# Performance work log

Hardware: AMD Instinct MI355X
Metric: run time of the kernel (lower is better)

## Reference

```python
import jax, jax.numpy as jnp
import numpy as np

N = 100000   # nodes
E = 1600000  # edges
F = 128      # n_feat
HID = 64     # n_hid
L = 4        # n_layer
C = 40       # n_class
TEMP = 0.1   # summarize temperature


def setup_inputs() -> dict:
    key = jax.random.key(0)
    ks = jax.random.split(key, 10)
    x = jax.random.normal(ks[0], (N, F), dtype=jnp.float32)
    edge_index = jax.random.randint(ks[1], (2, E), 0, N, dtype=jnp.int64)
    s_in = 1.0 / np.sqrt(F)
    s_h = 1.0 / np.sqrt(HID)
    W0 = jax.random.normal(ks[2], (F, HID), dtype=jnp.float32) * s_in
    b0 = jnp.zeros((HID,), dtype=jnp.float32)
    Ws = jax.random.normal(ks[3], (L - 1, HID, HID), dtype=jnp.float32) * s_h
    bs = jnp.zeros((L - 1, HID), dtype=jnp.float32)
    Wq = jax.random.normal(ks[4], (HID, HID), dtype=jnp.float32) * s_h
    Wk = jax.random.normal(ks[5], (HID, HID), dtype=jnp.float32) * s_h
    Wout = jax.random.normal(ks[6], (HID, C), dtype=jnp.float32) * s_h
    bout = jnp.zeros((C,), dtype=jnp.float32)
    return {"x": x, "edge_index": edge_index, "W0": W0, "b0": b0,
            "Ws": Ws, "bs": bs, "Wq": Wq, "Wk": Wk, "Wout": Wout, "bout": bout}


def reference(x, edge_index, W0, b0, Ws, bs, Wq, Wk, Wout, bout):
    # --- GCN normalization with self-loops (symmetric D^-1/2 (A+I) D^-1/2) ---
    loop = jnp.arange(N, dtype=edge_index.dtype)
    src = jnp.concatenate([edge_index[0], loop])  # [E+N]
    dst = jnp.concatenate([edge_index[1], loop])
    deg = jax.ops.segment_sum(jnp.ones_like(dst, dtype=x.dtype), dst, num_segments=N)
    dinv = jnp.where(deg > 0, jax.lax.rsqrt(deg), 0.0)
    enorm = dinv[src] * dinv[dst]  # [E+N]

    def propagate(h):
        # gather -> scale -> scatter-add (sparse matvec)
        msg = h[src] * enorm[:, None]
        return jax.ops.segment_sum(msg, dst, num_segments=N)

    # --- twin-branch stacked GCN convs (x_ starts as detached copy; eval mode => no dropout) ---
    h, h_ = x, x
    hs, hs_ = [], []
    for l in range(L):
        W = W0 if l == 0 else Ws[l - 1]
        b = b0 if l == 0 else bs[l - 1]
        h = jax.nn.relu(propagate(h @ W) + b)
        h_ = jax.nn.relu(propagate(h_ @ W) + b)
        hs.append(h)
        hs_.append(h_)

    Hm = jnp.stack(hs)    # [L, N, HID]
    Hm_ = jnp.stack(hs_)  # [L, N, HID]

    # --- Summarize: per-node attention over layer scales; query from twin branch ---
    q = jnp.einsum('lnd,de->lne', Hm_, Wq)
    k = jnp.einsum('lnd,de->lne', Hm, Wk)
    scores = jnp.sum(q * k, axis=-1) / TEMP      # [L, N]
    att = jax.nn.softmax(scores, axis=0)         # softmax over layers
    hsum = jnp.einsum('ln,lnd->nd', att, Hm)     # [N, HID]

    return hsum @ Wout + bout                    # [N, C]
```

## Files before the change

kernel.cpp:

```cpp
#include <hip/hip_runtime.h>
#include <hip/hip_bf16.h>
#include <math.h>

#define NN 100000
#define EE 1600000
#define FF 128
#define HH 64
#define CC 40

constexpr int SCAN_B = 1024;
constexpr int NB = (NN + SCAN_B - 1) / SCAN_B;

constexpr int RN = NN / 8;
constexpr int BCAP = 220000;
constexpr int NE_BLK = 2000;
constexpr int ABLK = EE / NE_BLK;
constexpr int GBLK = 64;
constexpr int SELFB2 = (RN + GBLK - 1) / GBLK;

__global__ void k_init(int* __restrict__ deg, int* __restrict__ bcnt) {
    int i = blockIdx.x * 256 + threadIdx.x;
    if (i < NN) deg[i] = 1;
    if (i < 8) bcnt[i] = 0;
}

__global__ __launch_bounds__(256) void k_bucket(const int* __restrict__ ei, int* __restrict__ bcnt,
                                                int* __restrict__ bsrc, int* __restrict__ bdst) {
    __shared__ int lcnt[8], lbase[8], loff[8];
    const int t = threadIdx.x;
    if (t < 8) { lcnt[t] = 0; loff[t] = 0; }
    __syncthreads();
    const int e0 = blockIdx.x * NE_BLK;
    int es[8], ed[8];
    int kmax = 0;
#pragma unroll
    for (int k = 0; k < 8; ++k) {
        int e = e0 + t + k * 256;
        if (t + k * 256 < NE_BLK) {
            es[k] = ei[e];
            ed[k] = ei[EE + e];
            atomicAdd(&lcnt[ed[k] / RN], 1);
            kmax = k + 1;
        }
    }
    __syncthreads();
    if (t < 8) lbase[t] = atomicAdd(&bcnt[t], lcnt[t]);
    __syncthreads();
#pragma unroll
    for (int k = 0; k < 8; ++k) {
        if (k < kmax) {
            int b = ed[k] / RN;
            int pos = lbase[b] + atomicAdd(&loff[b], 1);
            if (pos < BCAP) {
                bsrc[b * BCAP + pos] = es[k];
                bdst[b * BCAP + pos] = ed[k];
            }
        }
    }
}

__global__ void k_count2(const int* __restrict__ bdst, const int* __restrict__ bcnt,
                         int* __restrict__ deg) {
    const int g = blockIdx.x & 7;
    const int j = blockIdx.x >> 3;
    const int cnt = bcnt[g];
    const int* __restrict__ dp = bdst + g * BCAP;
    for (int i = j * 256 + threadIdx.x; i < cnt; i += GBLK * 256) {
        atomicAdd(&deg[dp[i]], 1);
    }
}

__global__ void k_dinv(const int* __restrict__ deg, float* __restrict__ dinv) {
    int i = blockIdx.x * 256 + threadIdx.x;
    if (i < NN) dinv[i] = rsqrtf((float)deg[i]);
}

__global__ void k_scanA(const int* __restrict__ deg, int* __restrict__ excl, int* __restrict__ bsum) {
    __shared__ int s[SCAN_B];
    int t = threadIdx.x;
    int g = blockIdx.x * SCAN_B + t;
    int v = (g < NN) ? deg[g] : 0;
    s[t] = v;
    __syncthreads();
    for (int o = 1; o < SCAN_B; o <<= 1) {
        int u = (t >= o) ? s[t - o] : 0;
        __syncthreads();
        s[t] += u;
        __syncthreads();
    }
    if (g < NN) excl[g] = s[t] - v;
    if (t == SCAN_B - 1) bsum[blockIdx.x] = s[t];
}

__global__ void k_scanB(int* __restrict__ bsum) {
    __shared__ int s[128];
    int t = threadIdx.x;
    int v = (t < NB) ? bsum[t] : 0;
    s[t] = v;
    __syncthreads();
    for (int o = 1; o < 128; o <<= 1) {
        int u = (t >= o) ? s[t - o] : 0;
        __syncthreads();
        s[t] += u;
        __syncthreads();
    }
    if (t < NB) bsum[t] = s[t] - v;
}

__global__ void k_scanC(int* __restrict__ rp, const int* __restrict__ bsum, int* __restrict__ cursor) {
    int t = threadIdx.x;
    int g = blockIdx.x * SCAN_B + t;
    if (g < NN) {
        int v = rp[g] + bsum[blockIdx.x];
        rp[g] = v;
        cursor[g] = v;
    }
    if (g == 0) rp[NN] = EE + NN;
}

__global__ void k_fill2(const int* __restrict__ bsrc, const int* __restrict__ bdst,
                        const int* __restrict__ bcnt, int* __restrict__ cursor, int* __restrict__ cs) {
    const int g = blockIdx.x & 7;
    const int j = blockIdx.x >> 3;
    const int cnt = bcnt[g];
    const int* __restrict__ sp = bsrc + g * BCAP;
    const int* __restrict__ dp = bdst + g * BCAP;
    for (int i = j * 256 + threadIdx.x; i < cnt; i += GBLK * 256) {
        int d = dp[i];
        int p = atomicAdd(&cursor[d], 1);
        cs[p] = sp[i];
    }
    const int lo = g * RN;
    int n = lo + j * SELFB2 + threadIdx.x;
    if (threadIdx.x < SELFB2 && n < lo + RN) {
        int p = atomicAdd(&cursor[n], 1);
        cs[p] = n;
    }
}

template <int K>
__global__ __launch_bounds__(256) void k_gemm(const float* __restrict__ A, const float* __restrict__ W,
                                              const float* __restrict__ dinv, float* __restrict__ Z,
                                              int nrows) {
    constexpr int S = 68;
    __shared__ float wl[64 * 64];
    __shared__ float hl[64 * S];
    const int t = threadIdx.x;
    const int r0 = blockIdx.x * 64;
    const int rg = t >> 4, cg = t & 15;
    float acc[4][4] = {};

    for (int kb = 0; kb < K; kb += 64) {
        {
            const float4* Wv = (const float4*)(W + kb * 64);
            for (int i = t; i < 1024; i += 256) ((float4*)wl)[i] = Wv[i];
        }
        for (int i = t; i < 1024; i += 256) {
            int row = i >> 4, d4 = i & 15;
            float4 v = {0.f, 0.f, 0.f, 0.f};
            if (r0 + row < nrows) v = *(const float4*)(A + (size_t)(r0 + row) * K + kb + d4 * 4);
            *(float4*)(hl + row * S + d4 * 4) = v;
        }
        __syncthreads();
#pragma unroll 8
        for (int d = 0; d < 64; ++d) {
            float4 w4 = *(const float4*)(wl + d * 64 + cg * 4);
#pragma unroll
            for (int i = 0; i < 4; i++) {
                float h = hl[(rg * 4 + i) * S + d];
                acc[i][0] = fmaf(h, w4.x, acc[i][0]);
                acc[i][1] = fmaf(h, w4.y, acc[i][1]);
                acc[i][2] = fmaf(h, w4.z, acc[i][2]);
                acc[i][3] = fmaf(h, w4.w, acc[i][3]);
            }
        }
        __syncthreads();
    }
#pragma unroll
    for (int i = 0; i < 4; i++) {
        int row = r0 + rg * 4 + i;
        if (row < nrows) {
            float dv = dinv[row];
            float4 o = {acc[i][0] * dv, acc[i][1] * dv, acc[i][2] * dv, acc[i][3] * dv};
            *(float4*)(Z + (size_t)row * 64 + cg * 4) = o;
        }
    }
}

__global__ __launch_bounds__(256) void k_prepM(const float* __restrict__ Wq, const float* __restrict__ Wk,
                                               float* __restrict__ M) {
    __shared__ float wk[64 * 65];
    __shared__ float wq[4 * 64];
    const int t = threadIdx.x;
    for (int i = t; i < 1024; i += 256) {
        int r = i >> 4, c4 = i & 15;
        float4 v = ((const float4*)Wk)[i];
        wk[r * 65 + c4 * 4 + 0] = v.x;
        wk[r * 65 + c4 * 4 + 1] = v.y;
        wk[r * 65 + c4 * 4 + 2] = v.z;
        wk[r * 65 + c4 * 4 + 3] = v.w;
    }
    const int rbase = blockIdx.x * 4;
    wq[t] = Wq[rbase * 64 + t];
    __syncthreads();
    const int rr = t >> 6;
    const int c = t & 63;
    float acc = 0.f;
#pragma unroll 8
    for (int e = 0; e < 64; ++e) acc = fmaf(wq[rr * 64 + e], wk[c * 65 + e], acc);
    M[(rbase + rr) * 64 + c] = acc;
}

__global__ __launch_bounds__(256) void k_score(const float* __restrict__ Hm, const float* __restrict__ M,
                                               float* __restrict__ scores) {
    constexpr int S = 68;
    __shared__ float wl[4096];
    __shared__ float hl[64 * S];
    const int t = threadIdx.x;
    const int r0 = blockIdx.x * 64;
    for (int i = t; i < 1024; i += 256) ((float4*)wl)[i] = ((const float4*)M)[i];
    for (int i = t; i < 1024; i += 256) {
        int row = i >> 4, d4 = i & 15;
        *(float4*)(hl + row * S + d4 * 4) = *(const float4*)(Hm + (size_t)(r0 + row) * 64 + d4 * 4);
    }
    __syncthreads();
    const int rg = t >> 4, cg = t & 15;
    float u[4][4] = {};
#pragma unroll 8
    for (int d = 0; d < 64; ++d) {
        float4 m4 = *(const float4*)(wl + d * 64 + cg * 4);
#pragma unroll
        for (int i = 0; i < 4; i++) {
            float h = hl[(rg * 4 + i) * S + d];
            u[i][0] = fmaf(h, m4.x, u[i][0]);
            u[i][1] = fmaf(h, m4.y, u[i][1]);
            u[i][2] = fmaf(h, m4.z, u[i][2]);
            u[i][3] = fmaf(h, m4.w, u[i][3]);
        }
    }
#pragma unroll
    for (int i = 0; i < 4; i++) {
        const float* hrow = hl + (rg * 4 + i) * S + cg * 4;
        float p = u[i][0] * hrow[0] + u[i][1] * hrow[1] + u[i][2] * hrow[2] + u[i][3] * hrow[3];
        p += __shfl_xor(p, 1);
        p += __shfl_xor(p, 2);
        p += __shfl_xor(p, 4);
        p += __shfl_xor(p, 8);
        if (cg == 0) scores[r0 + rg * 4 + i] = p;
    }
}

__global__ __launch_bounds__(256) void k_prop(const float* __restrict__ z, const int* __restrict__ rp,
                                              const int* __restrict__ cs, const float* __restrict__ dinv,
                                              const float* __restrict__ bias, float* __restrict__ out) {
    const int lane = threadIdx.x & 63;
    const int g = lane >> 4;
    const int l4 = lane & 15;
    const int n = blockIdx.x * 16 + (threadIdx.x >> 6) * 4 + g;
    const int beg = rp[n], end = rp[n + 1];
    float4 a0 = {0, 0, 0, 0}, a1 = {0, 0, 0, 0}, a2 = {0, 0, 0, 0}, a3 = {0, 0, 0, 0};
    int i = beg;
    for (; i + 8 <= end; i += 8) {
        int c0 = __builtin_nontemporal_load(cs + i);
        int c1 = __builtin_nontemporal_load(cs + i + 1);
        int c2 = __builtin_nontemporal_load(cs + i + 2);
        int c3 = __builtin_nontemporal_load(cs + i + 3);
        int c4 = __builtin_nontemporal_load(cs + i + 4);
        int c5 = __builtin_nontemporal_load(cs + i + 5);
        int c6 = __builtin_nontemporal_load(cs + i + 6);
        int c7 = __builtin_nontemporal_load(cs + i + 7);
        float4 z0 = *(const float4*)(z + (size_t)(unsigned)c0 * 64 + l4 * 4);
        float4 z1 = *(const float4*)(z + (size_t)(unsigned)c1 * 64 + l4 * 4);
        float4 z2 = *(const float4*)(z + (size_t)(unsigned)c2 * 64 + l4 * 4);
        float4 z3 = *(const float4*)(z + (size_t)(unsigned)c3 * 64 + l4 * 4);
        float4 z4 = *(const float4*)(z + (size_t)(unsigned)c4 * 64 + l4 * 4);
        float4 z5 = *(const float4*)(z + (size_t)(unsigned)c5 * 64 + l4 * 4);
        float4 z6 = *(const float4*)(z + (size_t)(unsigned)c6 * 64 + l4 * 4);
        float4 z7 = *(const float4*)(z + (size_t)(unsigned)c7 * 64 + l4 * 4);
        a0.x += z0.x; a0.y += z0.y; a0.z += z0.z; a0.w += z0.w;
        a1.x += z1.x; a1.y += z1.y; a1.z += z1.z; a1.w += z1.w;
        a2.x += z2.x; a2.y += z2.y; a2.z += z2.z; a2.w += z2.w;
        a3.x += z3.x; a3.y += z3.y; a3.z += z3.z; a3.w += z3.w;
        a0.x += z4.x; a0.y += z4.y; a0.z += z4.z; a0.w += z4.w;
        a1.x += z5.x; a1.y += z5.y; a1.z += z5.z; a1.w += z5.w;
        a2.x += z6.x; a2.y += z6.y; a2.z += z6.z; a2.w += z6.w;
        a3.x += z7.x; a3.y += z7.y; a3.z += z7.z; a3.w += z7.w;
    }
    for (; i + 4 <= end; i += 4) {
        int c0 = __builtin_nontemporal_load(cs + i);
        int c1 = __builtin_nontemporal_load(cs + i + 1);
        int c2 = __builtin_nontemporal_load(cs + i + 2);
        int c3 = __builtin_nontemporal_load(cs + i + 3);
        float4 z0 = *(const float4*)(z + (size_t)(unsigned)c0 * 64 + l4 * 4);
        float4 z1 = *(const float4*)(z + (size_t)(unsigned)c1 * 64 + l4 * 4);
        float4 z2 = *(const float4*)(z + (size_t)(unsigned)c2 * 64 + l4 * 4);
        float4 z3 = *(const float4*)(z + (size_t)(unsigned)c3 * 64 + l4 * 4);
        a0.x += z0.x; a0.y += z0.y; a0.z += z0.z; a0.w += z0.w;
        a1.x += z1.x; a1.y += z1.y; a1.z += z1.z; a1.w += z1.w;
        a2.x += z2.x; a2.y += z2.y; a2.z += z2.z; a2.w += z2.w;
        a3.x += z3.x; a3.y += z3.y; a3.z += z3.z; a3.w += z3.w;
    }
    for (; i < end; ++i) {
        int c = __builtin_nontemporal_load(cs + i);
        float4 zr = *(const float4*)(z + (size_t)(unsigned)c * 64 + l4 * 4);
        a0.x += zr.x; a0.y += zr.y; a0.z += zr.z; a0.w += zr.w;
    }
    const float dn = dinv[n];
    const float4 b4 = *(const float4*)(bias + l4 * 4);
    float4 r;
    r.x = fmaf(dn, (a0.x + a1.x) + (a2.x + a3.x), b4.x);
    r.y = fmaf(dn, (a0.y + a1.y) + (a2.y + a3.y), b4.y);
    r.z = fmaf(dn, (a0.z + a1.z) + (a2.z + a3.z), b4.z);
    r.w = fmaf(dn, (a0.w + a1.w) + (a2.w + a3.w), b4.w);
    r.x = r.x > 0.f ? r.x : 0.f;
    r.y = r.y > 0.f ? r.y : 0.f;
    r.z = r.z > 0.f ? r.z : 0.f;
    r.w = r.w > 0.f ? r.w : 0.f;
    *(float4*)(out + (size_t)n * 64 + l4 * 4) = r;
}

__global__ __launch_bounds__(256) void k_sum(const float* __restrict__ Hm, const float* __restrict__ scores,
                                             const float* __restrict__ Wout, const float* __restrict__ bout,
                                             float* __restrict__ out) {
    __shared__ float wo[64 * CC];
    __shared__ float hsl[4][64];
    const int t = threadIdx.x;
    for (int i = t; i < (64 * CC) / 4; i += 256) ((float4*)wo)[i] = ((const float4*)Wout)[i];
    __syncthreads();
    const int lane = t & 63;
    const int wid = t >> 6;
    const int n = blockIdx.x * 4 + wid;
    float h0 = Hm[(size_t)(0 * NN + n) * 64 + lane];
    float h1 = Hm[(size_t)(1 * NN + n) * 64 + lane];
    float h2 = Hm[(size_t)(2 * NN + n) * 64 + lane];
    float h3 = Hm[(size_t)(3 * NN + n) * 64 + lane];
    float s0 = scores[0 * NN + n] * 10.f;
    float s1 = scores[1 * NN + n] * 10.f;
    float s2 = scores[2 * NN + n] * 10.f;
    float s3 = scores[3 * NN + n] * 10.f;
    float m = fmaxf(fmaxf(s0, s1), fmaxf(s2, s3));
    float e0 = __expf(s0 - m), e1 = __expf(s1 - m), e2 = __expf(s2 - m), e3 = __expf(s3 - m);
    float inv = 1.f / (e0 + e1 + e2 + e3);
    float hs = (e0 * h0 + e1 * h1 + e2 * h2 + e3 * h3) * inv;
    hsl[wid][lane] = hs;
    float acc = 0.f;
#pragma unroll 8
    for (int d = 0; d < 64; ++d) {
        if (lane < CC) acc = fmaf(hsl[wid][d], wo[d * CC + lane], acc);
    }
    if (lane < CC) out[(size_t)n * CC + lane] = acc + bout[lane];
}

extern "C" void kernel_launch(void* const* d_in, const int* in_sizes, int n_in,
                              void* d_out, int out_size, void* d_ws, size_t ws_size,
                              hipStream_t stream) {
    const float* x    = (const float*)d_in[0];
    const int*   ei   = (const int*)d_in[1];
    const float* W0   = (const float*)d_in[2];
    const float* b0   = (const float*)d_in[3];
    const float* Ws   = (const float*)d_in[4];
    const float* bs   = (const float*)d_in[5];
    const float* Wq   = (const float*)d_in[6];
    const float* Wk   = (const float*)d_in[7];
    const float* Wout = (const float*)d_in[8];
    const float* bout = (const float*)d_in[9];
    float* out = (float*)d_out;

    char* p = (char*)d_ws;
    auto carve = [&](size_t bytes) {
        void* r = (void*)p;
        p += (bytes + 255) & ~(size_t)255;
        return r;
    };
    int*   deg     = (int*)carve((size_t)NN * 4);
    float* dinv    = (float*)carve((size_t)NN * 4);
    int*   row_ptr = (int*)carve((size_t)(NN + 1) * 4);
    int*   cursor  = (int*)carve((size_t)NN * 4);
    int*   bsum    = (int*)carve(256 * 4);
    int*   bcnt    = (int*)carve(8 * 4);
    int*   bsrc    = (int*)carve((size_t)8 * BCAP * 4);
    int*   bdst    = (int*)carve((size_t)8 * BCAP * 4);
    int*   cs      = (int*)carve((size_t)(EE + NN) * 4);
    float* M       = (float*)carve((size_t)HH * HH * 4);
    float* z       = (float*)carve((size_t)NN * HH * 4);
    float* Hm      = (float*)carve((size_t)4 * NN * HH * 4);
    float* scores  = (float*)carve((size_t)4 * NN * 4);
    (void)ws_size; (void)n_in; (void)in_sizes; (void)out_size;

    const int GB_N  = (NN + 255) / 256;
    const int GT    = (NN + 63) / 64;
    const int GSC   = (4 * NN) / 64;
    const int GP    = NN / 16;
    const int GS    = NN / 4;

    k_init<<<GB_N, 256, 0, stream>>>(deg, bcnt);
    k_bucket<<<ABLK, 256, 0, stream>>>(ei, bcnt, bsrc, bdst);
    k_count2<<<GBLK * 8, 256, 0, stream>>>(bdst, bcnt, deg);
    k_dinv<<<GB_N, 256, 0, stream>>>(deg, dinv);
    k_scanA<<<NB, SCAN_B, 0, stream>>>(deg, row_ptr, bsum);
    k_scanB<<<1, 128, 0, stream>>>(bsum);
    k_scanC<<<NB, SCAN_B, 0, stream>>>(row_ptr, bsum, cursor);
    k_fill2<<<GBLK * 8, 256, 0, stream>>>(bsrc, bdst, bcnt, cursor, cs);
    k_prepM<<<16, 256, 0, stream>>>(Wq, Wk, M);

    k_gemm<FF><<<GT, 256, 0, stream>>>(x, W0, dinv, z, NN);
    k_prop<<<GP, 256, 0, stream>>>(z, row_ptr, cs, dinv, b0, Hm);
    for (int l = 1; l < 4; ++l) {
        k_gemm<HH><<<GT, 256, 0, stream>>>(Hm + (size_t)(l - 1) * NN * HH,
                                           Ws + (size_t)(l - 1) * HH * HH, dinv, z, NN);
        k_prop<<<GP, 256, 0, stream>>>(z, row_ptr, cs, dinv, bs + (size_t)(l - 1) * HH,
                                       Hm + (size_t)l * NN * HH);
    }

    k_score<<<GSC, 256, 0, stream>>>(Hm, M, scores);
    k_sum<<<GS, 256, 0, stream>>>(Hm, scores, Wout, bout, out);
}
```

Before: 720.8 us.

## Pack bucket edges as 64-bit pairs, retile summarize kernel, nontemporal prop stores

Bucketed edges are now stored as packed 64-bit (src,dst) pairs, so the count and fill kernels each do a single load per edge. The count and fill kernels get twice as many blocks. The propagate output is written with nontemporal stores. The final summarize kernel now handles 64 nodes per block: softmax weights go to shared memory, then a vectorized weighted sum over layers, then a register-tiled output GEMV where each thread computes 10 classes. This cuts Wout reloads and idle lanes, but adds shared memory use and two barriers per block.

```diff
diff --git a/kernel.cpp b/kernel.cpp
--- a/kernel.cpp
+++ b/kernel.cpp
@@ -11,11 +11,14 @@
 constexpr int SCAN_B = 1024;
 constexpr int NB = (NN + SCAN_B - 1) / SCAN_B;
 
+typedef unsigned long long u64;
+typedef float f32x4 __attribute__((ext_vector_type(4)));
+
 constexpr int RN = NN / 8;
 constexpr int BCAP = 220000;
 constexpr int NE_BLK = 2000;
 constexpr int ABLK = EE / NE_BLK;
-constexpr int GBLK = 64;
+constexpr int GBLK = 128;
 constexpr int SELFB2 = (RN + GBLK - 1) / GBLK;
 
 __global__ void k_init(int* __restrict__ deg, int* __restrict__ bcnt) {
@@ -25,7 +28,7 @@
 }
 
 __global__ __launch_bounds__(256) void k_bucket(const int* __restrict__ ei, int* __restrict__ bcnt,
-                                                int* __restrict__ bsrc, int* __restrict__ bdst) {
+                                                u64* __restrict__ bpr) {
     __shared__ int lcnt[8], lbase[8], loff[8];
     const int t = threadIdx.x;
     if (t < 8) { lcnt[t] = 0; loff[t] = 0; }
@@ -52,21 +55,20 @@
             int b = ed[k] / RN;
             int pos = lbase[b] + atomicAdd(&loff[b], 1);
             if (pos < BCAP) {
-                bsrc[b * BCAP + pos] = es[k];
-                bdst[b * BCAP + pos] = ed[k];
+                bpr[(size_t)b * BCAP + pos] = (u64)(unsigned)es[k] | ((u64)(unsigned)ed[k] << 32);
             }
         }
     }
 }
 
-__global__ void k_count2(const int* __restrict__ bdst, const int* __restrict__ bcnt,
+__global__ void k_count2(const u64* __restrict__ bpr, const int* __restrict__ bcnt,
                          int* __restrict__ deg) {
     const int g = blockIdx.x & 7;
     const int j = blockIdx.x >> 3;
     const int cnt = bcnt[g];
-    const int* __restrict__ dp = bdst + g * BCAP;
+    const u64* __restrict__ pp = bpr + (size_t)g * BCAP;
     for (int i = j * 256 + threadIdx.x; i < cnt; i += GBLK * 256) {
-        atomicAdd(&deg[dp[i]], 1);
+        atomicAdd(&deg[(int)(pp[i] >> 32)], 1);
     }
 }
 
@@ -118,17 +120,17 @@
     if (g == 0) rp[NN] = EE + NN;
 }
 
-__global__ void k_fill2(const int* __restrict__ bsrc, const int* __restrict__ bdst,
-                        const int* __restrict__ bcnt, int* __restrict__ cursor, int* __restrict__ cs) {
+__global__ void k_fill2(const u64* __restrict__ bpr, const int* __restrict__ bcnt,
+                        int* __restrict__ cursor, int* __restrict__ cs) {
     const int g = blockIdx.x & 7;
     const int j = blockIdx.x >> 3;
     const int cnt = bcnt[g];
-    const int* __restrict__ sp = bsrc + g * BCAP;
-    const int* __restrict__ dp = bdst + g * BCAP;
+    const u64* __restrict__ pp = bpr + (size_t)g * BCAP;
     for (int i = j * 256 + threadIdx.x; i < cnt; i += GBLK * 256) {
-        int d = dp[i];
+        u64 u = pp[i];
+        int d = (int)(u >> 32);
         int p = atomicAdd(&cursor[d], 1);
-        cs[p] = sp[i];
+        cs[p] = (int)(unsigned)u;
     }
     const int lo = g * RN;
     int n = lo + j * SELFB2 + threadIdx.x;
@@ -316,39 +318,77 @@
     r.y = r.y > 0.f ? r.y : 0.f;
     r.z = r.z > 0.f ? r.z : 0.f;
     r.w = r.w > 0.f ? r.w : 0.f;
-    *(float4*)(out + (size_t)n * 64 + l4 * 4) = r;
+    __builtin_nontemporal_store(*(const f32x4*)&r, (f32x4*)(out + (size_t)n * 64 + l4 * 4));
 }
 
 __global__ __launch_bounds__(256) void k_sum(const float* __restrict__ Hm, const float* __restrict__ scores,
                                              const float* __restrict__ Wout, const float* __restrict__ bout,
                                              float* __restrict__ out) {
     __shared__ float wo[64 * CC];
-    __shared__ float hsl[4][64];
+    __shared__ float hs[64][68];
+    __shared__ float wl4[4][64];
     const int t = threadIdx.x;
+    const int r0 = blockIdx.x * 64;
     for (int i = t; i < (64 * CC) / 4; i += 256) ((float4*)wo)[i] = ((const float4*)Wout)[i];
-    __syncthreads();
-    const int lane = t & 63;
-    const int wid = t >> 6;
-    const int n = blockIdx.x * 4 + wid;
-    float h0 = Hm[(size_t)(0 * NN + n) * 64 + lane];
-    float h1 = Hm[(size_t)(1 * NN + n) * 64 + lane];
-    float h2 = Hm[(size_t)(2 * NN + n) * 64 + lane];
-    float h3 = Hm[(size_t)(3 * NN + n) * 64 + lane];
-    float s0 = scores[0 * NN + n] * 10.f;
-    float s1 = scores[1 * NN + n] * 10.f;
-    float s2 = scores[2 * NN + n] * 10.f;
-    float s3 = scores[3 * NN + n] * 10.f;
-    float m = fmaxf(fmaxf(s0, s1), fmaxf(s2, s3));
-    float e0 = __expf(s0 - m), e1 = __expf(s1 - m), e2 = __expf(s2 - m), e3 = __expf(s3 - m);
-    float inv = 1.f / (e0 + e1 + e2 + e3);
-    float hs = (e0 * h0 + e1 * h1 + e2 * h2 + e3 * h3) * inv;
-    hsl[wid][lane] = hs;
-    float acc = 0.f;
-#pragma unroll 8
+    if (t < 64) {
+        int n = r0 + t;
+        float s0 = 0.f, s1 = 0.f, s2 = 0.f, s3 = 0.f;
+        if (n < NN) {
+            s0 = scores[0 * NN + n] * 10.f;
+            s1 = scores[1 * NN + n] * 10.f;
+            s2 = scores[2 * NN + n] * 10.f;
+            s3 = scores[3 * NN + n] * 10.f;
+        }
+        float m = fmaxf(fmaxf(s0, s1), fmaxf(s2, s3));
+        float e0 = __expf(s0 - m), e1 = __expf(s1 - m), e2 = __expf(s2 - m), e3 = __expf(s3 - m);
+        float inv = 1.f / (e0 + e1 + e2 + e3);
+        wl4[0][t] = e0 * inv;
+        wl4[1][t] = e1 * inv;
+        wl4[2][t] = e2 * inv;
+        wl4[3][t] = e3 * inv;
+    }
+    __syncthreads();
+    for (int i = t; i < 1024; i += 256) {
+        int row = i >> 4, d4 = i & 15;
+        int n = r0 + row;
+        float4 acc = {0.f, 0.f, 0.f, 0.f};
+        if (n < NN) {
+#pragma unroll
+            for (int l = 0; l < 4; ++l) {
+                float w = wl4[l][row];
+                float4 h = *(const float4*)(Hm + ((size_t)l * NN + n) * 64 + d4 * 4);
+                acc.x = fmaf(w, h.x, acc.x);
+                acc.y = fmaf(w, h.y, acc.y);
+                acc.z = fmaf(w, h.z, acc.z);
+                acc.w = fmaf(w, h.w, acc.w);
+            }
+        }
+        *(float4*)(&hs[row][d4 * 4]) = acc;
+    }
+    __syncthreads();
+    const int row = t >> 2, cg = t & 3;
+    float2 acc2[5] = {};
     for (int d = 0; d < 64; ++d) {
-        if (lane < CC) acc = fmaf(hsl[wid][d], wo[d * CC + lane], acc);
-    }
-    if (lane < CC) out[(size_t)n * CC + lane] = acc + bout[lane];
+        float a = hs[row][d];
+        const float2* wrow = (const float2*)(wo + d * CC + cg * 10);
+#pragma unroll
+        for (int j = 0; j < 5; ++j) {
+            float2 w = wrow[j];
+            acc2[j].x = fmaf(a, w.x, acc2[j].x);
+            acc2[j].y = fmaf(a, w.y, acc2[j].y);
+        }
+    }
+    int n = r0 + row;
+    if (n < NN) {
+        float* op = out + (size_t)n * CC + cg * 10;
+        const float* bp = bout + cg * 10;
+#pragma unroll
+        for (int j = 0; j < 5; ++j) {
+            float2 b = *(const float2*)(bp + 2 * j);
+            float2 o = {acc2[j].x + b.x, acc2[j].y + b.y};
+            *(float2*)(op + 2 * j) = o;
+        }
+    }
 }
 
 extern "C" void kernel_launch(void* const* d_in, const int* in_sizes, int n_in,
@@ -378,8 +418,7 @@
     int*   cursor  = (int*)carve((size_t)NN * 4);
     int*   bsum    = (int*)carve(256 * 4);
     int*   bcnt    = (int*)carve(8 * 4);
-    int*   bsrc    = (int*)carve((size_t)8 * BCAP * 4);
-    int*   bdst    = (int*)carve((size_t)8 * BCAP * 4);
+    u64*   bpr     = (u64*)carve((size_t)8 * BCAP * 8);
     int*   cs      = (int*)carve((size_t)(EE + NN) * 4);
     float* M       = (float*)carve((size_t)HH * HH * 4);
     float* z       = (float*)carve((size_t)NN * HH * 4);
@@ -391,16 +430,16 @@
     const int GT    = (NN + 63) / 64;
     const int GSC   = (4 * NN) / 64;
     const int GP    = NN / 16;
-    const int GS    = NN / 4;
+    const int GS2   = (NN + 63) / 64;
 
     k_init<<<GB_N, 256, 0, stream>>>(deg, bcnt);
-    k_bucket<<<ABLK, 256, 0, stream>>>(ei, bcnt, bsrc, bdst);
-    k_count2<<<GBLK * 8, 256, 0, stream>>>(bdst, bcnt, deg);
+    k_bucket<<<ABLK, 256, 0, stream>>>(ei, bcnt, bpr);
+    k_count2<<<GBLK * 8, 256, 0, stream>>>(bpr, bcnt, deg);
     k_dinv<<<GB_N, 256, 0, stream>>>(deg, dinv);
     k_scanA<<<NB, SCAN_B, 0, stream>>>(deg, row_ptr, bsum);
     k_scanB<<<1, 128, 0, stream>>>(bsum);
     k_scanC<<<NB, SCAN_B, 0, stream>>>(row_ptr, bsum, cursor);
-    k_fill2<<<GBLK * 8, 256, 0, stream>>>(bsrc, bdst, bcnt, cursor, cs);
+    k_fill2<<<GBLK * 8, 256, 0, stream>>>(bpr, bcnt, cursor, cs);
     k_prepM<<<16, 256, 0, stream>>>(Wq, Wk, M);
 
     k_gemm<FF><<<GT, 256, 0, stream>>>(x, W0, dinv, z, NN);
@@ -413,5 +452,5 @@
     }
 
     k_score<<<GSC, 256, 0, stream>>>(Hm, M, scores);
-    k_sum<<<GS, 256, 0, stream>>>(Hm, scores, Wout, bout, out);
-}
+    k_sum<<<GS2, 256, 0, stream>>>(Hm, scores, Wout, bout, out);
+}
```

After: 695.6 us. 3.5% less time.
